# Optimization experiments

Measured on AMD Instinct MI355X. Metric: run time of the kernel, lower is better.

The kernel has to match this reference:

```python
import jax, jax.numpy as jnp
import numpy as np

EPS = 1e-5  # torch BatchNorm default eps


def _bn(x, gamma, beta, axes):
    # training-mode batch norm over `axes` (channel axis is 1), biased variance as in torch
    mean = x.mean(axis=axes, keepdims=True)
    var = x.var(axis=axes, keepdims=True)
    shp = [1] * x.ndim
    shp[1] = -1
    return gamma.reshape(shp) * (x - mean) * jax.lax.rsqrt(var + EPS) + beta.reshape(shp)


def setup_inputs() -> dict:
    key = jax.random.key(0)
    k0, k1, k2 = jax.random.split(key, 3)
    B, C, H, W = 4, 64, 128, 128
    OP2 = 128      # out_planes * 2
    HEAD = 8       # head_dim
    HP = OP2 // HEAD  # head_planes = 16
    return {
        "x": jax.random.normal(k0, (B, C, H, W), jnp.float32),
        "w_qkv": jax.random.normal(k1, (OP2, C), jnp.float32) / np.sqrt(C).astype(np.float32),
        "gamma1": jnp.ones((OP2,), jnp.float32),
        "beta1": jnp.zeros((OP2,), jnp.float32),
        "pos_relative": jax.random.normal(k2, (HP, 2 * H - 1), jnp.float32) / np.sqrt(C).astype(np.float32),
        "gate_qr": jnp.array([0.1], jnp.float32),
        "gate_kr": jnp.array([0.1], jnp.float32),
        "gate_v_pos": jnp.array([0.1], jnp.float32),
        "gate_v": jnp.array([1.0], jnp.float32),
        "gamma_att": jnp.ones((3 * HEAD,), jnp.float32),
        "beta_att": jnp.zeros((3 * HEAD,), jnp.float32),
        "gamma_v": jnp.ones((2 * HEAD,), jnp.float32),
        "beta_v": jnp.zeros((2 * HEAD,), jnp.float32),
    }


def reference(x, w_qkv, gamma1, beta1, pos_relative, gate_qr, gate_kr,
              gate_v_pos, gate_v, gamma_att, beta_att, gamma_v, beta_v):
    b, c, H, W = x.shape
    # h_w='h': permute [0,3,1,2] -> (b, W, c, H), fuse (b, W)
    xp = jnp.transpose(x, (0, 3, 1, 2)).reshape(b * W, c, H)  # [N, c, H]
    # to_qkv: 1x1 Conv1d (no bias) + ReLU + BatchNorm1d (training mode)
    y = jax.nn.relu(jnp.einsum('oc,ncl->nol', w_qkv, xp))      # [N, 2*out_planes, H]
    y = _bn(y, gamma1, beta1, (0, 2))

    head_dim = gamma_att.shape[0] // 3
    hp = y.shape[1] // head_dim          # head_planes
    qk_dim = hp // 4
    v_dim = hp // 2
    qkv = y.reshape(-1, head_dim, hp, H)  # [N, head_dim, head_planes, H]
    q = qkv[:, :, :qk_dim]
    k = qkv[:, :, qk_dim:2 * qk_dim]
    v = qkv[:, :, 2 * qk_dim:]

    # relative-position gather: pos_relative[:, q_idx - k_idx + H - 1] -> [head_planes, H, H]
    rel = jnp.arange(H)[:, None] - jnp.arange(H)[None, :] + H - 1
    qk_pos = pos_relative[:, rel]
    q_pos = qk_pos[:qk_dim]
    k_pos = qk_pos[qk_dim:2 * qk_dim]
    v_pos = qk_pos[2 * qk_dim:]

    qk = jnp.einsum('nhcp,nhci->nhpi', q, k)                 # [N, head_dim, H, H]
    qr = jnp.einsum('nhcp,cpi->nhpi', q, q_pos) * gate_qr
    kr = jnp.einsum('nhcp,cpi->nhpi', k, k_pos) * gate_kr

    att = _bn(jnp.concatenate([qk, qr, kr], axis=1), gamma_att, beta_att, (0, 2, 3))
    att = att.reshape(-1, 3, head_dim, H, H).sum(axis=1)
    att = jax.nn.softmax(att, axis=-1)

    att_v = jnp.einsum('nhpi,nhci->nhcp', att, v * gate_v)          # [N, head_dim, v_dim, H]
    att_vp = jnp.einsum('nhpi,cpi->nhcp', att, v_pos * gate_v_pos)

    z = _bn(jnp.concatenate([att_v, att_vp], axis=1), gamma_v, beta_v, (0, 2, 3))
    z = z.reshape(b, W, 2, head_dim * v_dim, H).sum(axis=2)  # [b, W, out_planes, H]
    # h_w='h': permute [0,2,3,1] -> (b, out_planes, H, W)
    return jnp.transpose(z, (0, 2, 3, 1))
```

## Files before the change

kernel.cpp:

```cpp
#include <hip/hip_runtime.h>
#include <hip/hip_fp16.h>

#define EPS 1e-5f



typedef _Float16 half2_t __attribute__((ext_vector_type(2)));

__device__ __constant__ int pair_c [10] = {0,0,0,0,1,1,1,2,2,3};
__device__ __constant__ int pair_cp[10] = {0,1,2,3,1,2,3,2,3,3};

__device__ inline float fdot2(half2_t a, half2_t b, float c) {
#if __has_builtin(__builtin_amdgcn_fdot2)
  return __builtin_amdgcn_fdot2(a, b, c, false);
#else
  return c + (float)a[0] * (float)b[0] + (float)a[1] * (float)b[1];
#endif
}
__device__ inline half2_t bch2(unsigned u) {
  union { unsigned u; half2_t h; } x; x.u = u; return x.h;
}
__device__ inline unsigned bcu(half2_t h) {
  union { unsigned u; half2_t h; } x; x.h = h; return x.u;
}
__device__ inline unsigned packf2(float a, float b) {
  half2_t h; h[0] = (_Float16)a; h[1] = (_Float16)b;
  union { unsigned u; half2_t h; } x; x.h = h; return x.u;
}
__device__ inline unsigned pkmul(unsigned u, half2_t c) {
  return bcu(bch2(u) * c);
}

__global__ __launch_bounds__(256) void k1_gemm(
    const float* __restrict__ x, const float* __restrict__ wq,
    _Float16* __restrict__ y1h, float* __restrict__ Pbuf)
{
  __shared__ float xs[64][132];
  const int b = blockIdx.x >> 7, l = blockIdx.x & 127;
  const int tid = threadIdx.x;
  const float* xp = x + (size_t)b * 1048576 + (size_t)l * 128;
  for (int idx = tid; idx < 2048; idx += 256) {
    int c = idx >> 5, w4 = (idx & 31) * 4;
    *(float4*)&xs[c][w4] = *(const float4*)&xp[c * 16384 + w4];
  }
  __syncthreads();
  const int ty = tid >> 4, tx = tid & 15;
  const int o0 = ty * 8, w0 = tx * 4;
  float acc[8][8];
#pragma unroll
  for (int u = 0; u < 8; ++u)
#pragma unroll
    for (int v = 0; v < 8; ++v) acc[u][v] = 0.f;

  for (int c4 = 0; c4 < 64; c4 += 4) {
    float wr[8][4];
#pragma unroll
    for (int u = 0; u < 8; ++u)
      *(float4*)&wr[u][0] = *(const float4*)&wq[(o0 + u) * 64 + c4];
#pragma unroll
    for (int dc = 0; dc < 4; ++dc) {
      float4 xa = *(const float4*)&xs[c4 + dc][w0];
      float4 xb = *(const float4*)&xs[c4 + dc][w0 + 64];
#pragma unroll
      for (int u = 0; u < 8; ++u) {
        float wv = wr[u][dc];
        acc[u][0] += wv * xa.x; acc[u][1] += wv * xa.y;
        acc[u][2] += wv * xa.z; acc[u][3] += wv * xa.w;
        acc[u][4] += wv * xb.x; acc[u][5] += wv * xb.y;
        acc[u][6] += wv * xb.z; acc[u][7] += wv * xb.w;
      }
    }
  }
  _Float16* y1p = y1h + (size_t)(b * 128 + l) * 16384;
#pragma unroll
  for (int u = 0; u < 8; ++u) {
#pragma unroll
    for (int v = 0; v < 8; ++v) acc[u][v] = fmaxf(acc[u][v], 0.f);
    uint2 pa, pb;
    pa.x = packf2(acc[u][0], acc[u][1]); pa.y = packf2(acc[u][2], acc[u][3]);
    pb.x = packf2(acc[u][4], acc[u][5]); pb.y = packf2(acc[u][6], acc[u][7]);
    *(uint2*)&y1p[(o0 + u) * 128 + w0] = pa;
    *(uint2*)&y1p[(o0 + u) * 128 + w0 + 64] = pb;
    float s  = acc[u][0] + acc[u][1] + acc[u][2] + acc[u][3]
             + acc[u][4] + acc[u][5] + acc[u][6] + acc[u][7];
    float ss = acc[u][0]*acc[u][0] + acc[u][1]*acc[u][1] + acc[u][2]*acc[u][2]
             + acc[u][3]*acc[u][3] + acc[u][4]*acc[u][4] + acc[u][5]*acc[u][5]
             + acc[u][6]*acc[u][6] + acc[u][7]*acc[u][7];
#pragma unroll
    for (int off = 1; off < 16; off <<= 1) {
      s  += __shfl_xor(s, off);
      ss += __shfl_xor(ss, off);
    }
    if (tx == 0) {
      Pbuf[blockIdx.x * 256 + o0 + u] = s;
      Pbuf[blockIdx.x * 256 + 128 + o0 + u] = ss;
    }
  }
}

__global__ __launch_bounds__(256) void k_tr(
    const _Float16* __restrict__ y1h, const float* __restrict__ Pbuf,
    const float* __restrict__ g1, const float* __restrict__ b1,
    unsigned* __restrict__ y2h)
{
  __shared__ _Float16 th[2][64][134];
  __shared__ float scsh[4];
  const int s = blockIdx.x & 63, b = blockIdx.x >> 6;
  const int h = s >> 3, slot = s & 7;
  const int o0 = 2 * s, o1 = 2 * s + 1;
  const int tid = threadIdx.x;
  {
    int r = tid >> 6, lane = tid & 63;
    int row = ((r & 1) ? o1 : o0) + (r >> 1) * 128;
    float a = 0.f;
#pragma unroll
    for (int m = 0; m < 8; ++m) a += Pbuf[(lane + 64 * m) * 256 + row];
#pragma unroll
    for (int off = 1; off < 64; off <<= 1) a += __shfl_xor(a, off);
    if (lane == 0) scsh[r] = a;
  }
  __syncthreads();
  const float inv = 1.f / 65536.f;
  const float m0 = scsh[0] * inv, v0 = scsh[2] * inv - m0 * m0;
  const float m1 = scsh[1] * inv, v1 = scsh[3] * inv - m1 * m1;
  const float sc0 = g1[o0] * rsqrtf(v0 + EPS), sh0 = b1[o0] - m0 * sc0;
  const float sc1 = g1[o1] * rsqrtf(v1 + EPS), sh1 = b1[o1] - m1 * sc1;
  for (int lh = 0; lh < 2; ++lh) {
    const int l0 = lh * 64;
    for (int idx = tid; idx < 4096; idx += 256) {
      int ll = idx >> 6, wp = idx & 63;
      size_t base = ((size_t)(b * 128 + l0 + ll) * 128) * 128 + 2 * wp;
      unsigned a0 = *(const unsigned*)&y1h[base + (size_t)o0 * 128];
      unsigned a1 = *(const unsigned*)&y1h[base + (size_t)o1 * 128];
      half2_t ha = bch2(a0), hb = bch2(a1);
      *(unsigned*)&th[0][ll][2 * wp] =
          packf2((float)ha[0] * sc0 + sh0, (float)ha[1] * sc0 + sh0);
      *(unsigned*)&th[1][ll][2 * wp] =
          packf2((float)hb[0] * sc1 + sh1, (float)hb[1] * sc1 + sh1);
    }
    __syncthreads();
    for (int idx = tid; idx < 8192; idx += 256) {
      int w = idx >> 6, ll = idx & 63;
      unsigned pk;
      { half2_t hh; hh[0] = th[0][ll][w]; hh[1] = th[1][ll][w];
        union { unsigned u; half2_t h; } xx; xx.h = hh; pk = xx.u; }
      y2h[((size_t)((b * 128 + w) * 8 + h) * 8 + slot) * 128 + l0 + ll] = pk;
    }
    __syncthreads();
  }
}

__global__ __launch_bounds__(128) void k0_pos(const float* __restrict__ pos,
                                              float* __restrict__ PT,
                                              unsigned* __restrict__ pos_h,
                                              unsigned* __restrict__ vpxg)
{
  const int blk = blockIdx.x, tid = threadIdx.x;
  if (blk == 28) {
    for (int u = tid; u < 255; u += 128) {
#pragma unroll
      for (int s = 0; s < 4; ++s)
        pos_h[u * 4 + s] = packf2(pos[(2 * s) * 255 + u], pos[(2 * s + 1) * 255 + u]);
    }
    return;
  }
  if (blk == 29) {
    for (int m = tid; m < 3084; m += 128) {
      int sel = m / 1540, rem = m - sel * 1540;
      unsigned val = 0;
      if (sel < 2 && rem < 1536) {
        int rp = rem / 12, c = rem % 12;
        if (c < 8) {
          int ua = (sel ? 254 : 253) - 2 * rp;
          int ub = ua - 1;
          float fa = (ua >= 0) ? pos[(8 + c) * 255 + ua] : 0.f;
          float fb = (ub >= 0) ? pos[(8 + c) * 255 + ub] : 0.f;
          val = packf2(fa, fb);
        }
      }
      vpxg[m] = val;
    }
    return;
  }
  __shared__ float r0[255], r1[255];
  int rowA, rowB, out;
  bool prod;
  if (blk < 4)       { rowA = blk;                 rowB = rowA;               out = blk * 128;              prod = false; }
  else if (blk < 14) { int m = blk - 4;  rowA = pair_c[m];     rowB = pair_cp[m];     out = 1024 + m * 128; prod = true; }
  else if (blk < 18) { rowA = 4 + (blk - 14);      rowB = rowA;               out = 512 + (blk - 14) * 128; prod = false; }
  else               { int m = blk - 18; rowA = 4 + pair_c[m]; rowB = 4 + pair_cp[m]; out = 2304 + m * 128; prod = true; }
  for (int u = tid; u < 255; u += 128) {
    r0[u] = pos[rowA * 255 + u];
    r1[u] = pos[rowB * 255 + u];
  }
  __syncthreads();
  float s = 0.f;
  if (prod) {
    for (int d = 0; d < 128; ++d) s += r0[tid + d] * r1[tid + d];
  } else {
    for (int d = 0; d < 128; ++d) s += r0[tid + d];
  }
  PT[out + tid] = s;
}

__global__ __launch_bounds__(256) void k3_stats(
    const unsigned* __restrict__ y2h, const float* __restrict__ PT,
    float* __restrict__ Pb3)
{
  const int W = blockIdx.x * 4 + (threadIdx.x >> 6);
  const int lane = threadIdx.x & 63;
  const unsigned* yb = y2h + (size_t)W * 1024;
  float q[4][2], k[4][2];
#pragma unroll
  for (int pl = 0; pl < 2; ++pl) {
    half2_t ha = bch2(yb[pl * 128 + lane]);
    half2_t hb = bch2(yb[pl * 128 + 64 + lane]);
    q[2 * pl][0] = (float)ha[0]; q[2 * pl + 1][0] = (float)ha[1];
    q[2 * pl][1] = (float)hb[0]; q[2 * pl + 1][1] = (float)hb[1];
    half2_t hc = bch2(yb[(2 + pl) * 128 + lane]);
    half2_t hd = bch2(yb[(2 + pl) * 128 + 64 + lane]);
    k[2 * pl][0] = (float)hc[0]; k[2 * pl + 1][0] = (float)hc[1];
    k[2 * pl][1] = (float)hd[0]; k[2 * pl + 1][1] = (float)hd[1];
  }
  float vals[32];
#pragma unroll
  for (int c = 0; c < 4; ++c) {
    vals[c]     = q[c][0] + q[c][1];
    vals[4 + c] = k[c][0] + k[c][1];
  }
#pragma unroll
  for (int m = 0; m < 10; ++m) {
    int c = pair_c[m], cp = pair_cp[m];
    vals[8 + m]  = q[c][0] * q[cp][0] + q[c][1] * q[cp][1];
    vals[18 + m] = k[c][0] * k[cp][0] + k[c][1] * k[cp][1];
  }
  float qr = 0, qrss = 0, kr = 0, krss = 0;
#pragma unroll
  for (int c = 0; c < 4; ++c) {
    qr += q[c][0] * PT[c * 128 + lane]       + q[c][1] * PT[c * 128 + 64 + lane];
    kr += k[c][0] * PT[512 + c * 128 + lane] + k[c][1] * PT[512 + c * 128 + 64 + lane];
  }
#pragma unroll
  for (int m = 0; m < 10; ++m) {
    int c = pair_c[m], cp = pair_cp[m];
    float mult = (c == cp) ? 1.f : 2.f;
    qrss += mult * (q[c][0] * q[cp][0] * PT[1024 + m * 128 + lane]
                  + q[c][1] * q[cp][1] * PT[1024 + m * 128 + 64 + lane]);
    krss += mult * (k[c][0] * k[cp][0] * PT[2304 + m * 128 + lane]
                  + k[c][1] * k[cp][1] * PT[2304 + m * 128 + 64 + lane]);
  }
  vals[28] = qr; vals[29] = qrss; vals[30] = kr; vals[31] = krss;
#pragma unroll
  for (int v = 0; v < 32; ++v) {
    float t = vals[v];
#pragma unroll
    for (int off = 1; off < 64; off <<= 1) t += __shfl_xor(t, off);
    vals[v] = t;
  }
  if (lane == 0) {
    float qk_sum = 0, qk_ss = 0;
#pragma unroll
    for (int c = 0; c < 4; ++c) qk_sum += vals[c] * vals[4 + c];
#pragma unroll
    for (int m = 0; m < 10; ++m) {
      float mult = (pair_c[m] == pair_cp[m]) ? 1.f : 2.f;
      qk_ss += mult * vals[8 + m] * vals[18 + m];
    }
    float* o = Pb3 + W * 6;
    o[0] = qk_sum; o[1] = qk_ss;
    o[2] = vals[28]; o[3] = vals[29]; o[4] = vals[30]; o[5] = vals[31];
  }
}

__global__ __launch_bounds__(384) void kR1(
    const float* __restrict__ Pb3, float* __restrict__ S,
    const float* __restrict__ ga, const float* __restrict__ ba,
    const float* __restrict__ gqr, const float* __restrict__ gkr)
{
  __shared__ float sums[48];
  const int t = threadIdx.x;
  const int col = t >> 3, sub = t & 7;
  if (col < 48) {
    const int h = col / 6, k = col % 6;
    float v = 0.f;
#pragma unroll
    for (int j = 0; j < 64; ++j) {
      int n = sub * 64 + j;
      v += Pb3[(size_t)(n * 8 + h) * 6 + k];
    }
    v += __shfl_xor(v, 1);
    v += __shfl_xor(v, 2);
    v += __shfl_xor(v, 4);
    if (sub == 0) sums[col] = v;
  }
  __syncthreads();
  if (t < 8) {
    const int h = t;
    const float inv = 1.f / 8388608.f;
    float gates[3] = {1.f, gqr[0], gkr[0]};
    float csum = 0.f;
#pragma unroll
    for (int g = 0; g < 3; ++g) {
      float mr = sums[h * 6 + 2 * g] * inv;
      float er = sums[h * 6 + 2 * g + 1] * inv;
      float gt = gates[g];
      float mean = gt * mr;
      float var = gt * gt * er - mean * mean;
      float sc = ga[g * 8 + h] * rsqrtf(var + EPS);
      S[560 + g * 8 + h] = gt * sc;
      csum += ba[g * 8 + h] - mean * sc;
    }
    S[584 + h] = csum;
  }
}

__global__ __launch_bounds__(512, 6) void k5_apply(
    const unsigned* __restrict__ y2h, const unsigned* __restrict__ pos_h,
    const unsigned* __restrict__ vpxg,
    float* __restrict__ S, _Float16* __restrict__ av, _Float16* __restrict__ avp,
    const float* __restrict__ gv_p, const float* __restrict__ gvp_p,
    float* __restrict__ Vbuf)
{
  __shared__ __align__(16) unsigned qkv_s[128][8];
  __shared__ __align__(16) unsigned posm[255][4];
  __shared__ __align__(16) unsigned vt[64][8];
  __shared__ __align__(16) unsigned vpxf[3084];
  __shared__ float red[8][4];
  const int h = blockIdx.x & 7, n = blockIdx.x >> 3;
  const int tid = threadIdx.x;
  const unsigned* yb = y2h + (size_t)(n * 8 + h) * 1024;
  const float C0 = S[560 + h], C1 = S[568 + h], C2 = S[576 + h], C3v = S[584 + h];
  half2_t C0h, C1h, C2h;
  C0h[0] = C0h[1] = (_Float16)C0;
  C1h[0] = C1h[1] = (_Float16)C1;
  C2h[0] = C2h[1] = (_Float16)C2;
  {
    int l = tid >> 2, s = tid & 3;
    if (s == 0) {
      unsigned q01 = yb[l], q23 = yb[128 + l];
      qkv_s[l][0] = pkmul(q01, C0h); qkv_s[l][1] = pkmul(q23, C0h);
    } else if (s == 1) {
      unsigned q01 = yb[l], q23 = yb[128 + l];
      qkv_s[l][2] = pkmul(q01, C1h); qkv_s[l][3] = pkmul(q23, C1h);
    } else if (s == 2) {
      qkv_s[l][4] = yb[256 + l]; qkv_s[l][5] = yb[384 + l];
    } else {
      qkv_s[l][6] = pkmul(yb[256 + l], C2h); qkv_s[l][7] = pkmul(yb[384 + l], C2h);
    }
  }
  {
    unsigned* pf = (unsigned*)posm;
    for (int m = tid; m < 1020; m += 512) pf[m] = pos_h[m];
  }
  for (int m = tid; m < 3084; m += 512) vpxf[m] = vpxg[m];
  if (tid < 256) {
    int s = tid & 3, jp = tid >> 2;
    unsigned a0 = yb[(4 + s) * 128 + 2 * jp];
    unsigned a1 = yb[(4 + s) * 128 + 2 * jp + 1];
    vt[jp][2 * s]     = (a0 & 0xffffu) | (a1 << 16);
    vt[jp][2 * s + 1] = (a0 >> 16) | (a1 & 0xffff0000u);
  }
  __syncthreads();

  const int p = tid >> 2, isub = tid & 3;
  uint4 qown = *(const uint4*)&qkv_s[p][0];
  uint2 kco  = *(const uint2*)&qkv_s[p][6];
  const half2_t qa01 = bch2(qown.x), qa23 = bch2(qown.y);
  const half2_t qb01 = bch2(qown.z), qb23 = bch2(qown.w);
  const half2_t kc01 = bch2(kco.x),  kc23 = bch2(kco.y);
  const unsigned* vprow = &vpxf[(p & 1) * 1540 + (63 - (p >> 1)) * 12];
  const half2_t one2 = bch2(packf2(1.f, 1.f));

  float mcur = -1e30f;
  float sum = 0.f;
  float accv[8], accvp[8];
#pragma unroll
  for (int c = 0; c < 8; ++c) { accv[c] = 0.f; accvp[c] = 0.f; }

#pragma unroll
  for (int jj = 0; jj < 8; ++jj) {
    const int jpA = isub + 8 * jj;
    const int jpB = jpA + 4;
    const int i0A = 2 * jpA, i0B = 2 * jpB;
    const int uA = p - i0A + 127;
    const int uB = uA - 8;
    uint2 kaA = *(const uint2*)&qkv_s[i0A][4];
    uint2 kbA = *(const uint2*)&qkv_s[i0A + 1][4];
    uint2 kaB = *(const uint2*)&qkv_s[i0B][4];
    uint2 kbB = *(const uint2*)&qkv_s[i0B + 1][4];
    uint4 paA = *(const uint4*)&posm[uA][0];
    uint4 pbA = *(const uint4*)&posm[uA - 1][0];
    uint4 paB = *(const uint4*)&posm[uB][0];
    uint4 pbB = *(const uint4*)&posm[uB - 1][0];
    float s0 = fdot2(qa01, bch2(kaA.x), fdot2(qa23, bch2(kaA.y),
               fdot2(qb01, bch2(paA.x), fdot2(qb23, bch2(paA.y),
               fdot2(kc01, bch2(paA.z), fdot2(kc23, bch2(paA.w), C3v))))));
    float s1 = fdot2(qa01, bch2(kbA.x), fdot2(qa23, bch2(kbA.y),
               fdot2(qb01, bch2(pbA.x), fdot2(qb23, bch2(pbA.y),
               fdot2(kc01, bch2(pbA.z), fdot2(kc23, bch2(pbA.w), C3v))))));
    float s2 = fdot2(qa01, bch2(kaB.x), fdot2(qa23, bch2(kaB.y),
               fdot2(qb01, bch2(paB.x), fdot2(qb23, bch2(paB.y),
               fdot2(kc01, bch2(paB.z), fdot2(kc23, bch2(paB.w), C3v))))));
    float s3 = fdot2(qa01, bch2(kbB.x), fdot2(qa23, bch2(kbB.y),
               fdot2(qb01, bch2(pbB.x), fdot2(qb23, bch2(pbB.y),
               fdot2(kc01, bch2(pbB.z), fdot2(kc23, bch2(pbB.w), C3v))))));
    float mp = fmaxf(fmaxf(s0, s1), fmaxf(s2, s3));
    if (mp > mcur) {
      float r = __expf(mcur - mp);
      mcur = mp;
      sum *= r;
#pragma unroll
      for (int c = 0; c < 8; ++c) { accv[c] *= r; accvp[c] *= r; }
    }
    float e0 = __expf(s0 - mcur);
    float e1 = __expf(s1 - mcur);
    float e2f = __expf(s2 - mcur);
    float e3f = __expf(s3 - mcur);
    const half2_t eA = bch2(packf2(e0, e1));
    const half2_t eB = bch2(packf2(e2f, e3f));
    sum = fdot2(eB, one2, fdot2(eA, one2, sum));
    uint4 vaA = *(const uint4*)&vt[jpA][0];
    uint4 vbA = *(const uint4*)&vt[jpA][4];
    uint4 vaB = *(const uint4*)&vt[jpB][0];
    uint4 vbB = *(const uint4*)&vt[jpB][4];
    const unsigned* wrA = vprow + jpA * 12;
    const unsigned* wrB = vprow + jpB * 12;
    uint4 waA = *(const uint4*)wrA;
    uint4 wbA = *(const uint4*)(wrA + 4);
    uint4 waB = *(const uint4*)wrB;
    uint4 wbB = *(const uint4*)(wrB + 4);
    accv[0] = fdot2(eB, bch2(vaB.x), fdot2(eA, bch2(vaA.x), accv[0]));
    accv[1] = fdot2(eB, bch2(vaB.y), fdot2(eA, bch2(vaA.y), accv[1]));
    accv[2] = fdot2(eB, bch2(vaB.z), fdot2(eA, bch2(vaA.z), accv[2]));
    accv[3] = fdot2(eB, bch2(vaB.w), fdot2(eA, bch2(vaA.w), accv[3]));
    accv[4] = fdot2(eB, bch2(vbB.x), fdot2(eA, bch2(vbA.x), accv[4]));
    accv[5] = fdot2(eB, bch2(vbB.y), fdot2(eA, bch2(vbA.y), accv[5]));
    accv[6] = fdot2(eB, bch2(vbB.z), fdot2(eA, bch2(vbA.z), accv[6]));
    accv[7] = fdot2(eB, bch2(vbB.w), fdot2(eA, bch2(vbA.w), accv[7]));
    accvp[0] = fdot2(eB, bch2(waB.x), fdot2(eA, bch2(waA.x), accvp[0]));
    accvp[1] = fdot2(eB, bch2(waB.y), fdot2(eA, bch2(waA.y), accvp[1]));
    accvp[2] = fdot2(eB, bch2(waB.z), fdot2(eA, bch2(waA.z), accvp[2]));
    accvp[3] = fdot2(eB, bch2(waB.w), fdot2(eA, bch2(waA.w), accvp[3]));
    accvp[4] = fdot2(eB, bch2(wbB.x), fdot2(eA, bch2(wbA.x), accvp[4]));
    accvp[5] = fdot2(eB, bch2(wbB.y), fdot2(eA, bch2(wbA.y), accvp[5]));
    accvp[6] = fdot2(eB, bch2(wbB.z), fdot2(eA, bch2(wbA.z), accvp[6]));
    accvp[7] = fdot2(eB, bch2(wbB.w), fdot2(eA, bch2(wbA.w), accvp[7]));
  }
  float M = fmaxf(mcur, __shfl_xor(mcur, 1));
  M = fmaxf(M, __shfl_xor(M, 2));
  {
    float r = __expf(mcur - M);
    sum *= r;
#pragma unroll
    for (int c = 0; c < 8; ++c) { accv[c] *= r; accvp[c] *= r; }
  }
  sum += __shfl_xor(sum, 1);
  sum += __shfl_xor(sum, 2);
#pragma unroll
  for (int c = 0; c < 8; ++c) {
    accv[c]  += __shfl_xor(accv[c], 1);  accv[c]  += __shfl_xor(accv[c], 2);
    accvp[c] += __shfl_xor(accvp[c], 1); accvp[c] += __shfl_xor(accvp[c], 2);
  }

  float sv = 0, ssv = 0, svp = 0, ssvp = 0;
  if (isub == 0) {
    const float fv = gv_p[0] / sum, fp2 = gvp_p[0] / sum;
    size_t base = ((size_t)(n * 8 + h) * 8) * 128 + p;
#pragma unroll
    for (int c = 0; c < 8; ++c) {
      float x1 = accv[c] * fv;
      float x2 = accvp[c] * fp2;
      av [base + c * 128] = (_Float16)x1;
      avp[base + c * 128] = (_Float16)x2;
      sv += x1; ssv += x1 * x1; svp += x2; ssvp += x2 * x2;
    }
  }
  float vals[4] = {sv, ssv, svp, ssvp};
#pragma unroll
  for (int kk = 0; kk < 4; ++kk) {
    float v = vals[kk];
#pragma unroll
    for (int off = 1; off < 64; off <<= 1) v += __shfl_xor(v, off);
    vals[kk] = v;
  }
  const int wid = tid >> 6, lane = tid & 63;
  if (lane == 0) {
#pragma unroll
    for (int kk = 0; kk < 4; ++kk) red[wid][kk] = vals[kk];
  }
  __syncthreads();
  if (tid == 0) {
    float t0 = 0, t1 = 0, t2 = 0, t3 = 0;
#pragma unroll
    for (int w = 0; w < 8; ++w) {
      t0 += red[w][0]; t1 += red[w][1]; t2 += red[w][2]; t3 += red[w][3];
    }
    float* o = Vbuf + (size_t)blockIdx.x * 4;
    o[0] = t0; o[1] = t1; o[2] = t2; o[3] = t3;
  }
}

__global__ __launch_bounds__(512) void kR2(
    const float* __restrict__ Vbuf, float* __restrict__ S,
    const float* __restrict__ gv, const float* __restrict__ bv)
{
  __shared__ float part[32][17];
  const int t = threadIdx.x;
  const int col = t >> 4, sub = t & 15;
  const int k = col >> 3, h = col & 7;
  float v = 0.f;
  for (int m = 0; m < 32; ++m) {
    int n = sub + 16 * m;
    v += Vbuf[(size_t)(n * 8 + h) * 4 + k];
  }
  part[col][sub] = v;
  __syncthreads();
  if (t < 32) {
    float s = 0.f;
#pragma unroll
    for (int j = 0; j < 16; ++j) s += part[t][j];
    part[t][16] = s;
  }
  __syncthreads();
  if (t < 8) {
    const int hh = t;
    const float inv = 1.f / 524288.f;
    float m1 = part[0 * 8 + hh][16] * inv;
    float e1 = part[1 * 8 + hh][16] * inv;
    float var = e1 - m1 * m1;
    float sc = gv[hh] * rsqrtf(var + EPS);
    S[624 + hh] = sc;
    S[632 + hh] = bv[hh] - m1 * sc;
    float m2 = part[2 * 8 + hh][16] * inv;
    float e2 = part[3 * 8 + hh][16] * inv;
    var = e2 - m2 * m2;
    sc = gv[8 + hh] * rsqrtf(var + EPS);
    S[640 + hh] = sc;
    S[648 + hh] = bv[8 + hh] - m2 * sc;
  }
}

__global__ __launch_bounds__(256) void k7_out(
    const _Float16* __restrict__ av, const _Float16* __restrict__ avp,
    const float* __restrict__ S, float* __restrict__ out)
{
  __shared__ float tile[64][129];
  const int wt = blockIdx.x & 1;
  const int d  = (blockIdx.x >> 1) & 63;
  const int b  = blockIdx.x >> 7;
  const int h = d >> 3, c = d & 7;
  const float scv = S[624 + h], shv = S[632 + h];
  const float scp = S[640 + h], shp = S[648 + h];
  const int tid = threadIdx.x;
  for (int idx = tid; idx < 8192; idx += 256) {
    int wl = idx >> 7, pp = idx & 127;
    int n = b * 128 + wt * 64 + wl;
    size_t base = (((size_t)n * 8 + h) * 8 + c) * 128 + pp;
    tile[wl][pp] = (float)av[base] * scv + shv + (float)avp[base] * scp + shp;
  }
  __syncthreads();
  for (int idx = tid; idx < 8192; idx += 256) {
    int pp = idx >> 6, wl = idx & 63;
    out[(((size_t)b * 64 + d) * 128 + pp) * 128 + wt * 64 + wl] = tile[wl][pp];
  }
}

extern "C" void kernel_launch(void* const* d_in, const int* in_sizes, int n_in,
                              void* d_out, int out_size, void* d_ws, size_t ws_size,
                              hipStream_t stream)
{
  const float* x   = (const float*)d_in[0];
  const float* wq  = (const float*)d_in[1];
  const float* g1  = (const float*)d_in[2];
  const float* b1  = (const float*)d_in[3];
  const float* pos = (const float*)d_in[4];
  const float* gqr = (const float*)d_in[5];
  const float* gkr = (const float*)d_in[6];
  const float* gvp = (const float*)d_in[7];
  const float* gv  = (const float*)d_in[8];
  const float* ga  = (const float*)d_in[9];
  const float* ba  = (const float*)d_in[10];
  const float* gv2 = (const float*)d_in[11];
  const float* bv2 = (const float*)d_in[12];

  float* ws = (float*)d_ws;
  _Float16* y1h   = (_Float16*)ws;
  _Float16* av    = (_Float16*)ws;
  _Float16* avp   = (_Float16*)ws + 4194304;
  float*    Pb3   = ws + 4200000;
  float*    Vbuf  = ws + 4250000;
  float*    Pbuf  = ws + 4300000;
  unsigned* y2h   = (unsigned*)(ws + 8388608);
  float*    S     = ws + 16777216;
  unsigned* pos_h = (unsigned*)(ws + 16778240);
  float*    PT    = ws + 16781312;
  unsigned* vpxg  = (unsigned*)(ws + 16785000);
  float*    out   = (float*)d_out;

  k0_pos<<<30, 128, 0, stream>>>(pos, PT, pos_h, vpxg);
  k1_gemm<<<512, 256, 0, stream>>>(x, wq, y1h, Pbuf);
  k_tr<<<256, 256, 0, stream>>>(y1h, Pbuf, g1, b1, y2h);
  k3_stats<<<1024, 256, 0, stream>>>(y2h, PT, Pb3);
  kR1<<<1, 384, 0, stream>>>(Pb3, S, ga, ba, gqr, gkr);
  k5_apply<<<4096, 512, 0, stream>>>(y2h, pos_h, vpxg, S, av, avp, gv, gvp, Vbuf);
  kR2<<<1, 512, 0, stream>>>(Vbuf, S, gv2, bv2);
  k7_out<<<512, 256, 0, stream>>>(av, avp, S, out);
}
```

Baseline: 175.6 us.

## Use fp16 dot2 in qkv projection GEMM and re-layout k5 shared buffers

The first GEMM kernel now stages x in shared memory as packed fp16 channel pairs and computes the 1x1 conv with fdot2 instead of fp32 FMAs. This halves shared-memory footprint and load traffic and the number of multiply instructions, at the cost of fp16 rounding of inputs and weights before batch norm. In the attention kernel, the position table is split into separate q and k arrays and the qkv and v tiles are padded to a stride of 12 words. The padding and split are meant to reduce LDS bank conflicts on the strided reads.

```diff
diff --git a/kernel.cpp b/kernel.cpp
--- a/kernel.cpp
+++ b/kernel.cpp
@@ -35,13 +35,18 @@
     const float* __restrict__ x, const float* __restrict__ wq,
     _Float16* __restrict__ y1h, float* __restrict__ Pbuf)
 {
-  __shared__ float xs[64][132];
+  __shared__ unsigned xs[32][132];
   const int b = blockIdx.x >> 7, l = blockIdx.x & 127;
   const int tid = threadIdx.x;
   const float* xp = x + (size_t)b * 1048576 + (size_t)l * 128;
-  for (int idx = tid; idx < 2048; idx += 256) {
-    int c = idx >> 5, w4 = (idx & 31) * 4;
-    *(float4*)&xs[c][w4] = *(const float4*)&xp[c * 16384 + w4];
+  for (int idx = tid; idx < 1024; idx += 256) {
+    int cp = idx >> 5, w4 = (idx & 31) * 4;
+    float4 r0 = *(const float4*)&xp[(2 * cp) * 16384 + w4];
+    float4 r1 = *(const float4*)&xp[(2 * cp + 1) * 16384 + w4];
+    uint4 o;
+    o.x = packf2(r0.x, r1.x); o.y = packf2(r0.y, r1.y);
+    o.z = packf2(r0.z, r1.z); o.w = packf2(r0.w, r1.w);
+    *(uint4*)&xs[cp][w4] = o;
   }
   __syncthreads();
   const int ty = tid >> 4, tx = tid & 15;
@@ -53,21 +58,31 @@
     for (int v = 0; v < 8; ++v) acc[u][v] = 0.f;
 
   for (int c4 = 0; c4 < 64; c4 += 4) {
-    float wr[8][4];
-#pragma unroll
-    for (int u = 0; u < 8; ++u)
-      *(float4*)&wr[u][0] = *(const float4*)&wq[(o0 + u) * 64 + c4];
-#pragma unroll
-    for (int dc = 0; dc < 4; ++dc) {
-      float4 xa = *(const float4*)&xs[c4 + dc][w0];
-      float4 xb = *(const float4*)&xs[c4 + dc][w0 + 64];
+    unsigned wr[8][2];
+#pragma unroll
+    for (int u = 0; u < 8; ++u) {
+      float4 wv = *(const float4*)&wq[(o0 + u) * 64 + c4];
+      wr[u][0] = packf2(wv.x, wv.y);
+      wr[u][1] = packf2(wv.z, wv.w);
+    }
+    const int cp0 = c4 >> 1;
+#pragma unroll
+    for (int d = 0; d < 2; ++d) {
+      uint4 xa = *(const uint4*)&xs[cp0 + d][w0];
+      uint4 xb = *(const uint4*)&xs[cp0 + d][w0 + 64];
+      half2_t a0 = bch2(xa.x), a1 = bch2(xa.y), a2 = bch2(xa.z), a3 = bch2(xa.w);
+      half2_t b0 = bch2(xb.x), b1 = bch2(xb.y), b2 = bch2(xb.z), b3 = bch2(xb.w);
 #pragma unroll
       for (int u = 0; u < 8; ++u) {
-        float wv = wr[u][dc];
-        acc[u][0] += wv * xa.x; acc[u][1] += wv * xa.y;
-        acc[u][2] += wv * xa.z; acc[u][3] += wv * xa.w;
-        acc[u][4] += wv * xb.x; acc[u][5] += wv * xb.y;
-        acc[u][6] += wv * xb.z; acc[u][7] += wv * xb.w;
+        half2_t wh = bch2(wr[u][d]);
+        acc[u][0] = fdot2(wh, a0, acc[u][0]);
+        acc[u][1] = fdot2(wh, a1, acc[u][1]);
+        acc[u][2] = fdot2(wh, a2, acc[u][2]);
+        acc[u][3] = fdot2(wh, a3, acc[u][3]);
+        acc[u][4] = fdot2(wh, b0, acc[u][4]);
+        acc[u][5] = fdot2(wh, b1, acc[u][5]);
+        acc[u][6] = fdot2(wh, b2, acc[u][6]);
+        acc[u][7] = fdot2(wh, b3, acc[u][7]);
       }
     }
   }
@@ -321,9 +336,10 @@
     const float* __restrict__ gv_p, const float* __restrict__ gvp_p,
     float* __restrict__ Vbuf)
 {
-  __shared__ __align__(16) unsigned qkv_s[128][8];
-  __shared__ __align__(16) unsigned posm[255][4];
-  __shared__ __align__(16) unsigned vt[64][8];
+  __shared__ __align__(16) unsigned qkv_s[128][12];
+  __shared__ __align__(8)  unsigned posq[256][2];
+  __shared__ __align__(8)  unsigned posk[256][2];
+  __shared__ __align__(16) unsigned vt[64][12];
   __shared__ __align__(16) unsigned vpxf[3084];
   __shared__ float red[8][4];
   const int h = blockIdx.x & 7, n = blockIdx.x >> 3;
@@ -348,9 +364,10 @@
       qkv_s[l][6] = pkmul(yb[256 + l], C2h); qkv_s[l][7] = pkmul(yb[384 + l], C2h);
     }
   }
-  {
-    unsigned* pf = (unsigned*)posm;
-    for (int m = tid; m < 1020; m += 512) pf[m] = pos_h[m];
+  if (tid < 255) {
+    uint4 t4 = *(const uint4*)&pos_h[tid * 4];
+    posq[tid][0] = t4.x; posq[tid][1] = t4.y;
+    posk[tid][0] = t4.z; posk[tid][1] = t4.w;
   }
   for (int m = tid; m < 3084; m += 512) vpxf[m] = vpxg[m];
   if (tid < 256) {
@@ -388,22 +405,26 @@
     uint2 kbA = *(const uint2*)&qkv_s[i0A + 1][4];
     uint2 kaB = *(const uint2*)&qkv_s[i0B][4];
     uint2 kbB = *(const uint2*)&qkv_s[i0B + 1][4];
-    uint4 paA = *(const uint4*)&posm[uA][0];
-    uint4 pbA = *(const uint4*)&posm[uA - 1][0];
-    uint4 paB = *(const uint4*)&posm[uB][0];
-    uint4 pbB = *(const uint4*)&posm[uB - 1][0];
+    uint2 pqA  = *(const uint2*)&posq[uA][0];
+    uint2 pqA1 = *(const uint2*)&posq[uA - 1][0];
+    uint2 pqB  = *(const uint2*)&posq[uB][0];
+    uint2 pqB1 = *(const uint2*)&posq[uB - 1][0];
+    uint2 pkA  = *(const uint2*)&posk[uA][0];
+    uint2 pkA1 = *(const uint2*)&posk[uA - 1][0];
+    uint2 pkB  = *(const uint2*)&posk[uB][0];
+    uint2 pkB1 = *(const uint2*)&posk[uB - 1][0];
     float s0 = fdot2(qa01, bch2(kaA.x), fdot2(qa23, bch2(kaA.y),
-               fdot2(qb01, bch2(paA.x), fdot2(qb23, bch2(paA.y),
-               fdot2(kc01, bch2(paA.z), fdot2(kc23, bch2(paA.w), C3v))))));
+               fdot2(qb01, bch2(pqA.x), fdot2(qb23, bch2(pqA.y),
+               fdot2(kc01, bch2(pkA.x), fdot2(kc23, bch2(pkA.y), C3v))))));
     float s1 = fdot2(qa01, bch2(kbA.x), fdot2(qa23, bch2(kbA.y),
-               fdot2(qb01, bch2(pbA.x), fdot2(qb23, bch2(pbA.y),
-               fdot2(kc01, bch2(pbA.z), fdot2(kc23, bch2(pbA.w), C3v))))));
+               fdot2(qb01, bch2(pqA1.x), fdot2(qb23, bch2(pqA1.y),
+               fdot2(kc01, bch2(pkA1.x), fdot2(kc23, bch2(pkA1.y), C3v))))));
     float s2 = fdot2(qa01, bch2(kaB.x), fdot2(qa23, bch2(kaB.y),
-               fdot2(qb01, bch2(paB.x), fdot2(qb23, bch2(paB.y),
-               fdot2(kc01, bch2(paB.z), fdot2(kc23, bch2(paB.w), C3v))))));
+               fdot2(qb01, bch2(pqB.x), fdot2(qb23, bch2(pqB.y),
+               fdot2(kc01, bch2(pkB.x), fdot2(kc23, bch2(pkB.y), C3v))))));
     float s3 = fdot2(qa01, bch2(kbB.x), fdot2(qa23, bch2(kbB.y),
-               fdot2(qb01, bch2(pbB.x), fdot2(qb23, bch2(pbB.y),
-               fdot2(kc01, bch2(pbB.z), fdot2(kc23, bch2(pbB.w), C3v))))));
+               fdot2(qb01, bch2(pqB1.x), fdot2(qb23, bch2(pqB1.y),
+               fdot2(kc01, bch2(pkB1.x), fdot2(kc23, bch2(pkB1.y), C3v))))));
     float mp = fmaxf(fmaxf(s0, s1), fmaxf(s2, s3));
     if (mp > mcur) {
       float r = __expf(mcur - mp);
```

After: 177.4 us. About the same (+1.0%).
